# Performance work log

Hardware: AMD Instinct MI355X
Metric: run time of the kernel (lower is better)

Reference implementation:

```python
import jax, jax.numpy as jnp
import numpy as np

D = 1024   # embed_dim
L = 8      # num_blocks
H = 8      # num_heads
T = 2048   # temporal length
DH = D // H


def _ln(x, g, b, eps):
    m = jnp.mean(x, axis=-1, keepdims=True)
    v = jnp.var(x, axis=-1, keepdims=True)
    return (x - m) * jax.lax.rsqrt(v + eps) * g + b


def setup_inputs() -> dict:
    key = jax.random.key(0)
    ks = iter(jax.random.split(key, 48))
    s = 0.02
    rn = lambda shape: jax.random.normal(next(ks), shape, jnp.float32) * s
    return {
        "video_features": jax.random.normal(next(ks), (1, T, 1024), jnp.float32),
        "audio_features": jax.random.normal(next(ks), (1, T, 128), jnp.float32),
        "ap_W1": rn((128, D // 2)), "ap_b1": jnp.zeros((D // 2,)),
        "ap_W2": rn((D // 2, D)), "ap_b2": jnp.zeros((D,)),
        "vp_W1": rn((1024, D // 2)), "vp_b1": jnp.zeros((D // 2,)),
        "vp_W2": rn((D // 2, D)), "vp_b2": jnp.zeros((D,)),
        "pre_ln_g": jnp.ones((D,)), "pre_ln_b": jnp.zeros((D,)),
        "blk_Wq": rn((L, D, D)), "blk_bq": jnp.zeros((L, D)),
        "blk_Wk": rn((L, D, D)), "blk_bk": jnp.zeros((L, D)),
        "blk_Wv": rn((L, D, D)), "blk_bv": jnp.zeros((L, D)),
        "blk_Wo": rn((L, D, D)), "blk_bo": jnp.zeros((L, D)),
        "blk_bias_k": rn((L, D)), "blk_bias_v": rn((L, D)),
        "blk_ln1_g": jnp.ones((L, D)), "blk_ln1_b": jnp.zeros((L, D)),
        "blk_ln2_g": jnp.ones((L, D)), "blk_ln2_b": jnp.zeros((L, D)),
        "blk_mW1": rn((L, D, 4 * D)), "blk_mb1": jnp.zeros((L, 4 * D)),
        "blk_mW2": rn((L, 4 * D, D)), "blk_mb2": jnp.zeros((L, D)),
        "lh_W1": rn((D, D // 2)), "lh_b1": jnp.zeros((D // 2,)),
        "lh_W2": rn((D // 2, 1)), "lh_b2": jnp.zeros((1,)),
        "threshold": jnp.float32(0.5),
    }


def reference(video_features, audio_features,
              ap_W1, ap_b1, ap_W2, ap_b2,
              vp_W1, vp_b1, vp_W2, vp_b2,
              pre_ln_g, pre_ln_b,
              blk_Wq, blk_bq, blk_Wk, blk_bk, blk_Wv, blk_bv, blk_Wo, blk_bo,
              blk_bias_k, blk_bias_v,
              blk_ln1_g, blk_ln1_b, blk_ln2_g, blk_ln2_b,
              blk_mW1, blk_mb1, blk_mW2, blk_mb2,
              lh_W1, lh_b1, lh_W2, lh_b2, threshold):
    # projectors (Linear -> ReLU -> Linear)
    a = jax.nn.relu(audio_features @ ap_W1 + ap_b1) @ ap_W2 + ap_b2   # [1,T,D]
    v = jax.nn.relu(video_features @ vp_W1 + vp_b1) @ vp_W2 + vp_b2   # [1,T,D]

    x = _ln(a, pre_ln_g, pre_ln_b, 1e-6)  # pre_transformer_layer LayerNorm

    def block(x, p):
        Wq, bq, Wk, bk, Wv, bv, Wo, bo, bkx, bvx, g1, b1, g2, b2, mW1, mb1, mW2, mb2 = p
        h = _ln(x, g1, b1, 1e-5)
        q = (h @ Wq + bq).reshape(1, T, H, DH)
        # cross K/V from projected video, plus the learned bias_k/bias_v token (add_bias_kv)
        k = jnp.concatenate([v @ Wk + bk, bkx[None, None, :]], axis=1).reshape(1, T + 1, H, DH)
        val = jnp.concatenate([v @ Wv + bv, bvx[None, None, :]], axis=1).reshape(1, T + 1, H, DH)
        scores = jnp.einsum('bthd,bshd->bhts', q, k) * (DH ** -0.5)   # [1,H,T,T+1]
        attn = jax.nn.softmax(scores, axis=-1)
        o = jnp.einsum('bhts,bshd->bthd', attn, val).reshape(1, T, D)
        x = x + o @ Wo + bo
        h2 = _ln(x, g2, b2, 1e-5)
        x = x + jax.nn.gelu(h2 @ mW1 + mb1) @ mW2 + mb2
        return x, None

    ps = (blk_Wq, blk_bq, blk_Wk, blk_bk, blk_Wv, blk_bv, blk_Wo, blk_bo,
          blk_bias_k, blk_bias_v, blk_ln1_g, blk_ln1_b, blk_ln2_g, blk_ln2_b,
          blk_mW1, blk_mb1, blk_mW2, blk_mb2)
    x, _ = jax.lax.scan(block, x, ps)

    # locate head: Linear -> ReLU -> Linear -> Sigmoid
    located = jax.nn.sigmoid(jax.nn.relu(x @ lh_W1 + lh_b1) @ lh_W2 + lh_b2)[..., 0]  # [1,T]

    # on-device run-length segmentation (replaces the per-step python loop)
    clips = (located[0] > threshold).astype(jnp.int32)                 # [T]
    seg_ids = jnp.concatenate([jnp.zeros((1,), jnp.int32),
                               jnp.cumsum((clips[1:] != clips[:-1]).astype(jnp.int32))])
    counts = jax.ops.segment_sum(jnp.ones((T,), jnp.float32), seg_ids, num_segments=T)
    denom = jnp.maximum(counts, 1.0)[:, None]
    # variable-length segment mean pooling (AdaptiveAvgPool1d(1) per segment), padded to T segments
    vid_pool = jax.ops.segment_sum(v[0], seg_ids, num_segments=T) / denom   # [T,D]
    aud_pool = jax.ops.segment_sum(a[0], seg_ids, num_segments=T) / denom   # [T,D]
    seg_types = jax.ops.segment_max(clips, seg_ids, num_segments=T)
    num_seg = seg_ids[-1] + 1
    return vid_pool[None], aud_pool[None], located, seg_ids, seg_types, num_seg
```

## Files before the change

### kernel.cpp

```cpp
#include <hip/hip_runtime.h>
#include <math.h>

typedef float4 f4;
typedef __attribute__((ext_vector_type(8))) short bf8v;
typedef __attribute__((ext_vector_type(4))) float f4v;

#define T_SEQ 2048
#define D_MOD 1024

__device__ __forceinline__ float gelu_f(float x){
    float u = 0.7978845608028654f*(x + 0.044715f*x*x*x);
    return 0.5f*x*(1.0f + tanhf(u));
}

__device__ __forceinline__ unsigned f32_to_pair(float x){
    unsigned u = __float_as_uint(x);
    unsigned hi = (u + 0x7FFFu + ((u >> 16) & 1u)) >> 16;
    float hif = __uint_as_float(hi << 16);
    float lof = x - hif;
    unsigned v = __float_as_uint(lof);
    unsigned lo = (v + 0x7FFFu + ((v >> 16) & 1u)) >> 16;
    return hi | (lo << 16);
}

__device__ __forceinline__ void split2(float x, short& hi, short& lo){
    unsigned u = __float_as_uint(x);
    hi = (short)(u >> 16);
    float rem = x - __uint_as_float(u & 0xFFFF0000u);
    lo = (short)(__float_as_uint(rem) >> 16);
}

__global__ __launch_bounds__(256) void convert1(
    const float* __restrict__ s, unsigned* __restrict__ d, int n4)
{
    const int i = blockIdx.x*256 + threadIdx.x;
    if (i < n4){
        f4 v = ((const f4*)s)[i];
        uint4 o;
        o.x = f32_to_pair(v.x); o.y = f32_to_pair(v.y);
        o.z = f32_to_pair(v.z); o.w = f32_to_pair(v.w);
        ((uint4*)d)[i] = o;
    }
}

__global__ __launch_bounds__(256) void convert6(
    const float* __restrict__ s0, const float* __restrict__ s1,
    const float* __restrict__ s2, const float* __restrict__ s3,
    const float* __restrict__ s4, const float* __restrict__ s5,
    unsigned* __restrict__ d0, unsigned* __restrict__ d1,
    unsigned* __restrict__ d2, unsigned* __restrict__ d3,
    unsigned* __restrict__ d4, unsigned* __restrict__ d5)
{
    const int stride = gridDim.x * 256;
    for (int idx = blockIdx.x*256 + threadIdx.x; idx < 3145728; idx += stride){
        const float* s; unsigned* d; int off;
        if (idx < 1048576){
            const int r = idx >> 18; off = idx & 262143;
            s = (r==0)?s0:(r==1)?s1:(r==2)?s2:s3;
            d = (r==0)?d0:(r==1)?d1:(r==2)?d2:d3;
        } else if (idx < 2097152){ s = s4; d = d4; off = idx - 1048576; }
        else                     { s = s5; d = d5; off = idx - 2097152; }
        f4 v = ((const f4*)s)[off];
        uint4 o;
        o.x = f32_to_pair(v.x); o.y = f32_to_pair(v.y);
        o.z = f32_to_pair(v.z); o.w = f32_to_pair(v.w);
        ((uint4*)d)[off] = o;
    }
}

__global__ __launch_bounds__(256) void gemm_mfma(
    const unsigned* __restrict__ Apr, const unsigned* __restrict__ Wpr,
    const float* __restrict__ bias, const float* __restrict__ res,
    float* __restrict__ Cf, unsigned* __restrict__ Cp,
    int M, int N, int K, int act, int hasres, int outpair)
{
    __shared__ short Ah[2][4][64][8];
    __shared__ short Al[2][4][64][8];
    __shared__ short Bh[2][8][64][8];
    __shared__ short Bl[2][8][64][8];
    const int tid = threadIdx.x;
    const int w = tid >> 6, l = tid & 63;
    const int row0 = blockIdx.y * 64, col0 = blockIdx.x * 128;
    const int mb = (w >> 1) * 2;
    const int nb = (w & 1) * 4;

    f4v acc[2][4];
    #pragma unroll
    for (int i=0;i<2;i++)
        #pragma unroll
        for (int j=0;j<4;j++) acc[i][j] = (f4v){0.f,0.f,0.f,0.f};

    const int b_c4 = (tid & 31) * 4;
    const int b_kg = tid >> 5;

    for (int k0 = 0; k0 < K; k0 += 64){
        if (k0) __syncthreads();
        #pragma unroll
        for (int i=0;i<2;i++){
            const int u = tid + i*256;
            const int ar = u >> 3, kg = u & 7;
            const unsigned* src = Apr + (size_t)(row0 + ar)*K + k0 + kg*8;
            const uint4 p0 = *(const uint4*)src;
            const uint4 p1 = *(const uint4*)(src + 4);
            bf8v hv, lv;
            hv[0]=(short)(p0.x); lv[0]=(short)(p0.x>>16);
            hv[1]=(short)(p0.y); lv[1]=(short)(p0.y>>16);
            hv[2]=(short)(p0.z); lv[2]=(short)(p0.z>>16);
            hv[3]=(short)(p0.w); lv[3]=(short)(p0.w>>16);
            hv[4]=(short)(p1.x); lv[4]=(short)(p1.x>>16);
            hv[5]=(short)(p1.y); lv[5]=(short)(p1.y>>16);
            hv[6]=(short)(p1.z); lv[6]=(short)(p1.z>>16);
            hv[7]=(short)(p1.w); lv[7]=(short)(p1.w>>16);
            const int lane = (ar & 15) | ((kg & 3) << 4);
            const int ks = kg >> 2, mf = ar >> 4;
            *(bf8v*)&Ah[ks][mf][lane][0] = hv;
            *(bf8v*)&Al[ks][mf][lane][0] = lv;
        }
        {
            uint4 r[8];
            #pragma unroll
            for (int j=0;j<8;j++)
                r[j] = *(const uint4*)(Wpr + (size_t)(k0 + b_kg*8 + j)*N + col0 + b_c4);
            #pragma unroll
            for (int c=0;c<4;c++){
                bf8v hv, lv;
                #pragma unroll
                for (int j=0;j<8;j++){
                    const unsigned e = ((const unsigned*)&r[j])[c];
                    hv[j] = (short)e; lv[j] = (short)(e >> 16);
                }
                const int col = b_c4 + c;
                const int lane = (col & 15) | ((b_kg & 3) << 4);
                const int ks = b_kg >> 2, nf = col >> 4;
                *(bf8v*)&Bh[ks][nf][lane][0] = hv;
                *(bf8v*)&Bl[ks][nf][lane][0] = lv;
            }
        }
        __syncthreads();
        #pragma unroll
        for (int ks=0; ks<2; ks++){
            const bf8v ah0 = *(const bf8v*)&Ah[ks][mb+0][l][0];
            const bf8v ah1 = *(const bf8v*)&Ah[ks][mb+1][l][0];
            const bf8v al0 = *(const bf8v*)&Al[ks][mb+0][l][0];
            const bf8v al1 = *(const bf8v*)&Al[ks][mb+1][l][0];
            #pragma unroll
            for (int nf=0; nf<4; nf++){
                const bf8v bh = *(const bf8v*)&Bh[ks][nb+nf][l][0];
                const bf8v bl = *(const bf8v*)&Bl[ks][nb+nf][l][0];
                acc[0][nf] = __builtin_amdgcn_mfma_f32_16x16x32_bf16(ah0, bh, acc[0][nf], 0,0,0);
                acc[0][nf] = __builtin_amdgcn_mfma_f32_16x16x32_bf16(ah0, bl, acc[0][nf], 0,0,0);
                acc[0][nf] = __builtin_amdgcn_mfma_f32_16x16x32_bf16(al0, bh, acc[0][nf], 0,0,0);
                acc[1][nf] = __builtin_amdgcn_mfma_f32_16x16x32_bf16(ah1, bh, acc[1][nf], 0,0,0);
                acc[1][nf] = __builtin_amdgcn_mfma_f32_16x16x32_bf16(ah1, bl, acc[1][nf], 0,0,0);
                acc[1][nf] = __builtin_amdgcn_mfma_f32_16x16x32_bf16(al1, bh, acc[1][nf], 0,0,0);
            }
        }
    }

    const int ecol = l & 15, erow = (l >> 4) * 4;
    #pragma unroll
    for (int mf=0; mf<2; mf++){
        #pragma unroll
        for (int nf=0; nf<4; nf++){
            const int col = col0 + (w&1)*64 + nf*16 + ecol;
            const float bv = bias[col];
            #pragma unroll
            for (int j=0; j<4; j++){
                const int row = row0 + (w>>1)*32 + mf*16 + erow + j;
                float v = acc[mf][nf][j] + bv;
                if (act==1) v = fmaxf(v, 0.f);
                else if (act==2) v = gelu_f(v);
                if (hasres) v += res[(size_t)row*N + col];
                if (outpair) Cp[(size_t)row*N + col] = f32_to_pair(v);
                else         Cf[(size_t)row*N + col] = v;
            }
        }
    }
}

__global__ __launch_bounds__(512) void gemm_mfma2(
    const unsigned* __restrict__ Apr, const unsigned* __restrict__ Wpr,
    const float* __restrict__ bias, const float* __restrict__ res,
    float* __restrict__ Cf, unsigned* __restrict__ Cp,
    int M, int N, int K, int act, int hasres, int outpair)
{
    __shared__ short Ah[2][2][4][64][8];
    __shared__ short Al[2][2][4][64][8];
    __shared__ short Bh[2][2][8][64][8];
    __shared__ short Bl[2][2][8][64][8];
    const int tid = threadIdx.x;
    const int kh = tid >> 8;
    const int t  = tid & 255;
    const int w = t >> 6, l = t & 63;
    int bx = blockIdx.x, by = blockIdx.y;
    if (gridDim.x == 8 && gridDim.y == 32){
        const int flat = by*8 + bx;
        by = (flat & 7)*4 + ((flat >> 3) & 3);
        bx = flat >> 5;
    }
    const int row0 = by * 64, col0 = bx * 128;
    const int mb = (w >> 1) * 2;
    const int nb = (w & 1) * 4;
    const int K2 = K >> 1;
    const int kbase = kh * K2;
    const int b_c4 = (t & 31) * 4;
    const int b_kg = t >> 5;
    const int a_r0 = t >> 3,       a_kg0 = t & 7;
    const int a_r1 = (t+256) >> 3, a_kg1 = (t+256) & 7;

    f4v acc[2][4];
    #pragma unroll
    for (int i=0;i<2;i++)
        #pragma unroll
        for (int j=0;j<4;j++) acc[i][j] = (f4v){0.f,0.f,0.f,0.f};

    uint4 pa0[2], pa1[2], pb[8];

    {
        const unsigned* s0 = Apr + (size_t)(row0 + a_r0)*K + kbase + a_kg0*8;
        const unsigned* s1 = Apr + (size_t)(row0 + a_r1)*K + kbase + a_kg1*8;
        pa0[0] = *(const uint4*)s0; pa0[1] = *(const uint4*)(s0+4);
        pa1[0] = *(const uint4*)s1; pa1[1] = *(const uint4*)(s1+4);
        #pragma unroll
        for (int j=0;j<8;j++)
            pb[j] = *(const uint4*)(Wpr + (size_t)(kbase + b_kg*8 + j)*N + col0 + b_c4);
    }

    #define STAGE_A(pr, ar, kg) { \
        bf8v hv, lv; \
        hv[0]=(short)(pr[0].x); lv[0]=(short)(pr[0].x>>16); \
        hv[1]=(short)(pr[0].y); lv[1]=(short)(pr[0].y>>16); \
        hv[2]=(short)(pr[0].z); lv[2]=(short)(pr[0].z>>16); \
        hv[3]=(short)(pr[0].w); lv[3]=(short)(pr[0].w>>16); \
        hv[4]=(short)(pr[1].x); lv[4]=(short)(pr[1].x>>16); \
        hv[5]=(short)(pr[1].y); lv[5]=(short)(pr[1].y>>16); \
        hv[6]=(short)(pr[1].z); lv[6]=(short)(pr[1].z>>16); \
        hv[7]=(short)(pr[1].w); lv[7]=(short)(pr[1].w>>16); \
        const int lane_ = ((ar) & 15) | (((kg) & 3) << 4); \
        *(bf8v*)&Ah[kh][(kg)>>2][(ar)>>4][lane_][0] = hv; \
        *(bf8v*)&Al[kh][(kg)>>2][(ar)>>4][lane_][0] = lv; }

    #define STAGE_B() { \
        _Pragma("unroll") \
        for (int c=0;c<4;c++){ \
            bf8v hv, lv; \
            _Pragma("unroll") \
            for (int j=0;j<8;j++){ \
                const unsigned e = ((const unsigned*)&pb[j])[c]; \
                hv[j] = (short)e; lv[j] = (short)(e >> 16); \
            } \
            const int col_ = b_c4 + c; \
            const int lane_ = (col_ & 15) | ((b_kg & 3) << 4); \
            *(bf8v*)&Bh[kh][b_kg>>2][col_>>4][lane_][0] = hv; \
            *(bf8v*)&Bl[kh][b_kg>>2][col_>>4][lane_][0] = lv; } }

    STAGE_A(pa0, a_r0, a_kg0)
    STAGE_A(pa1, a_r1, a_kg1)
    STAGE_B()
    __syncthreads();

    int k0 = 0;
    while (true){
        const int kn = k0 + 64;
        const bool more = kn < K2;
        if (more){
            const unsigned* s0 = Apr + (size_t)(row0 + a_r0)*K + kbase + kn + a_kg0*8;
            const unsigned* s1 = Apr + (size_t)(row0 + a_r1)*K + kbase + kn + a_kg1*8;
            pa0[0] = *(const uint4*)s0; pa0[1] = *(const uint4*)(s0+4);
            pa1[0] = *(const uint4*)s1; pa1[1] = *(const uint4*)(s1+4);
            #pragma unroll
            for (int j=0;j<8;j++)
                pb[j] = *(const uint4*)(Wpr + (size_t)(kbase + kn + b_kg*8 + j)*N + col0 + b_c4);
        }
        #pragma unroll
        for (int ks=0; ks<2; ks++){
            const bf8v ah0 = *(const bf8v*)&Ah[kh][ks][mb+0][l][0];
            const bf8v ah1 = *(const bf8v*)&Ah[kh][ks][mb+1][l][0];
            const bf8v al0 = *(const bf8v*)&Al[kh][ks][mb+0][l][0];
            const bf8v al1 = *(const bf8v*)&Al[kh][ks][mb+1][l][0];
            #pragma unroll
            for (int nf=0; nf<4; nf++){
                const bf8v bh = *(const bf8v*)&Bh[kh][ks][nb+nf][l][0];
                const bf8v bl = *(const bf8v*)&Bl[kh][ks][nb+nf][l][0];
                acc[0][nf] = __builtin_amdgcn_mfma_f32_16x16x32_bf16(ah0, bh, acc[0][nf], 0,0,0);
                acc[0][nf] = __builtin_amdgcn_mfma_f32_16x16x32_bf16(ah0, bl, acc[0][nf], 0,0,0);
                acc[0][nf] = __builtin_amdgcn_mfma_f32_16x16x32_bf16(al0, bh, acc[0][nf], 0,0,0);
                acc[1][nf] = __builtin_amdgcn_mfma_f32_16x16x32_bf16(ah1, bh, acc[1][nf], 0,0,0);
                acc[1][nf] = __builtin_amdgcn_mfma_f32_16x16x32_bf16(ah1, bl, acc[1][nf], 0,0,0);
                acc[1][nf] = __builtin_amdgcn_mfma_f32_16x16x32_bf16(al1, bh, acc[1][nf], 0,0,0);
            }
        }
        __syncthreads();
        if (!more) break;
        STAGE_A(pa0, a_r0, a_kg0)
        STAGE_A(pa1, a_r1, a_kg1)
        STAGE_B()
        __syncthreads();
        k0 = kn;
    }

    float* cs = (float*)&Ah[0][0][0][0][0];
    if (kh == 1){
        #pragma unroll
        for (int mf=0; mf<2; mf++)
            #pragma unroll
            for (int nf=0; nf<4; nf++){
                f4 p;
                p.x=acc[mf][nf][0]; p.y=acc[mf][nf][1];
                p.z=acc[mf][nf][2]; p.w=acc[mf][nf][3];
                *(f4*)(cs + 4*(((mf*4+nf))*256 + t)) = p;
            }
    }
    __syncthreads();
    if (kh == 0){
        #pragma unroll
        for (int mf=0; mf<2; mf++)
            #pragma unroll
            for (int nf=0; nf<4; nf++){
                const f4 p = *(const f4*)(cs + 4*(((mf*4+nf))*256 + t));
                acc[mf][nf][0]+=p.x; acc[mf][nf][1]+=p.y;
                acc[mf][nf][2]+=p.z; acc[mf][nf][3]+=p.w;
            }
        const int ecol = l & 15, erow = (l >> 4) * 4;
        #pragma unroll
        for (int mf=0; mf<2; mf++){
            #pragma unroll
            for (int nf=0; nf<4; nf++){
                const int col = col0 + (w&1)*64 + nf*16 + ecol;
                const float bv = bias[col];
                #pragma unroll
                for (int j=0; j<4; j++){
                    const int row = row0 + (w>>1)*32 + mf*16 + erow + j;
                    float v = acc[mf][nf][j] + bv;
                    if (act==1) v = fmaxf(v, 0.f);
                    else if (act==2) v = gelu_f(v);
                    if (hasres) v += res[(size_t)row*N + col];
                    if (outpair) Cp[(size_t)row*N + col] = f32_to_pair(v);
                    else         Cf[(size_t)row*N + col] = v;
                }
            }
        }
    }
    #undef STAGE_A
    #undef STAGE_B
}

__global__ __launch_bounds__(512) void gemm128k2(
    const float* __restrict__ A, const float* __restrict__ W,
    const float* __restrict__ bias, const float* __restrict__ res,
    float* __restrict__ C, int M, int N, int K, int act, int hasres)
{
    __shared__ float As[2][32][68];
    __shared__ float Ws[2][32][132];
    const int tid = threadIdx.x;
    const int kh = tid >> 8;
    const int t  = tid & 255;
    const int row0 = blockIdx.y*64, col0 = blockIdx.x*128;
    const int ty = t>>4, tx = t&15;
    const int am = t>>2, ak = (t&3)*8;
    const int wk = t>>3, u  = t&7;
    const int K2 = K >> 1;
    const float* Ap = A + (size_t)(row0+am)*K + kh*K2 + ak;
    const float* Wp = W + (size_t)(kh*K2 + wk)*N + col0 + u*16;
    float* Wrow = &Ws[kh][wk][0];

    f4 a0,a1,w0,w1,w2,w3;
    a0 = *(const f4*)(Ap);
    a1 = *(const f4*)(Ap + 4);
    w0 = *(const f4*)(Wp);
    w1 = *(const f4*)(Wp + 4);
    w2 = *(const f4*)(Wp + 8);
    w3 = *(const f4*)(Wp + 12);
    As[kh][ak+0][am]=a0.x; As[kh][ak+1][am]=a0.y; As[kh][ak+2][am]=a0.z; As[kh][ak+3][am]=a0.w;
    As[kh][ak+4][am]=a1.x; As[kh][ak+5][am]=a1.y; As[kh][ak+6][am]=a1.z; As[kh][ak+7][am]=a1.w;
    *(f4*)(Wrow + 8*u)      = w0;
    *(f4*)(Wrow + 8*u + 4)  = w2;
    *(f4*)(Wrow + 64 + 8*u)     = w1;
    *(f4*)(Wrow + 64 + 8*u + 4) = w3;
    __syncthreads();

    float acc[4][8];
    #pragma unroll
    for (int i=0;i<4;i++){
        #pragma unroll
        for (int j=0;j<8;j++) acc[i][j]=0.f;
    }

    int k0 = 0;
    while (true){
        const int kn = k0 + 32;
        const bool more = kn < K2;
        if (more){
            a0 = *(const f4*)(Ap + kn);
            a1 = *(const f4*)(Ap + kn + 4);
            w0 = *(const f4*)(Wp + (size_t)kn*N);
            w1 = *(const f4*)(Wp + (size_t)kn*N + 4);
            w2 = *(const f4*)(Wp + (size_t)kn*N + 8);
            w3 = *(const f4*)(Wp + (size_t)kn*N + 12);
        }
        #pragma unroll
        for (int kk=0;kk<32;kk++){
            f4 a  = *(const f4*)&As[kh][kk][ty*4];
            f4 wA = *(const f4*)&Ws[kh][kk][tx*4];
            f4 wB = *(const f4*)&Ws[kh][kk][64 + tx*4];
            float ar[4] = {a.x,a.y,a.z,a.w};
            #pragma unroll
            for (int i=0;i<4;i++){
                acc[i][0] += ar[i]*wA.x;
                acc[i][1] += ar[i]*wA.y;
                acc[i][2] += ar[i]*wA.z;
                acc[i][3] += ar[i]*wA.w;
                acc[i][4] += ar[i]*wB.x;
                acc[i][5] += ar[i]*wB.y;
                acc[i][6] += ar[i]*wB.z;
                acc[i][7] += ar[i]*wB.w;
            }
        }
        __syncthreads();
        if (!more) break;
        As[kh][ak+0][am]=a0.x; As[kh][ak+1][am]=a0.y; As[kh][ak+2][am]=a0.z; As[kh][ak+3][am]=a0.w;
        As[kh][ak+4][am]=a1.x; As[kh][ak+5][am]=a1.y; As[kh][ak+6][am]=a1.z; As[kh][ak+7][am]=a1.w;
        *(f4*)(Wrow + 8*u)      = w0;
        *(f4*)(Wrow + 8*u + 4)  = w2;
        *(f4*)(Wrow + 64 + 8*u)     = w1;
        *(f4*)(Wrow + 64 + 8*u + 4) = w3;
        __syncthreads();
        k0 = kn;
    }

    float* cs = &Ws[0][0][0];
    if (kh == 1){
        #pragma unroll
        for (int i=0;i<4;i++){
            #pragma unroll
            for (int b=0;b<2;b++){
                f4 p;
                p.x=acc[i][b*4+0]; p.y=acc[i][b*4+1]; p.z=acc[i][b*4+2]; p.w=acc[i][b*4+3];
                *(f4*)(cs + 4*(((i<<1)|b)*256 + t)) = p;
            }
        }
    }
    __syncthreads();
    if (kh == 0){
        #pragma unroll
        for (int i=0;i<4;i++){
            #pragma unroll
            for (int b=0;b<2;b++){
                const f4 p = *(const f4*)(cs + 4*(((i<<1)|b)*256 + t));
                acc[i][b*4+0]+=p.x; acc[i][b*4+1]+=p.y; acc[i][b*4+2]+=p.z; acc[i][b*4+3]+=p.w;
            }
        }
        #pragma unroll
        for (int i=0;i<4;i++){
            const int r = row0 + ty*4 + i;
            #pragma unroll
            for (int half=0; half<2; ++half){
                const int cb = col0 + tx*8 + half*4;
                f4 bv = *(const f4*)(bias + cb);
                float t0 = acc[i][half*4+0] + bv.x;
                float t1 = acc[i][half*4+1] + bv.y;
                float t2 = acc[i][half*4+2] + bv.z;
                float t3 = acc[i][half*4+3] + bv.w;
                if (act==1){ t0=fmaxf(t0,0.f); t1=fmaxf(t1,0.f); t2=fmaxf(t2,0.f); t3=fmaxf(t3,0.f); }
                else if (act==2){ t0=gelu_f(t0); t1=gelu_f(t1); t2=gelu_f(t2); t3=gelu_f(t3); }
                if (hasres){
                    f4 rv = *(const f4*)(res + (size_t)r*N + cb);
                    t0+=rv.x; t1+=rv.y; t2+=rv.z; t3+=rv.w;
                }
                f4 o; o.x=t0; o.y=t1; o.z=t2; o.w=t3;
                *(f4*)(C + (size_t)r*N + cb) = o;
            }
        }
    }
}

__global__ __launch_bounds__(256) void lnrow(
    const float* __restrict__ X, const float* __restrict__ g,
    const float* __restrict__ b, float* __restrict__ out, float eps)
{
    __shared__ float red[4];
    const int row = blockIdx.x, tid = threadIdx.x;
    const float* xp = X + (size_t)row*D_MOD;
    f4 xv = *(const f4*)(xp + tid*4);
    float s = xv.x+xv.y+xv.z+xv.w;
    #pragma unroll
    for (int m=1;m<64;m<<=1) s += __shfl_xor(s, m);
    const int wid = tid>>6, lane = tid&63;
    if (lane==0) red[wid]=s;
    __syncthreads();
    float mean = (red[0]+red[1]+red[2]+red[3]) * (1.0f/1024.0f);
    __syncthreads();
    float d0=xv.x-mean, d1=xv.y-mean, d2=xv.z-mean, d3=xv.w-mean;
    float q = d0*d0+d1*d1+d2*d2+d3*d3;
    #pragma unroll
    for (int m=1;m<64;m<<=1) q += __shfl_xor(q, m);
    if (lane==0) red[wid]=q;
    __syncthreads();
    float var = (red[0]+red[1]+red[2]+red[3]) * (1.0f/1024.0f);
    float inv = rsqrtf(var + eps);
    f4 gv = *(const f4*)(g + tid*4);
    f4 bv = *(const f4*)(b + tid*4);
    f4 o;
    o.x = d0*inv*gv.x + bv.x;
    o.y = d1*inv*gv.y + bv.y;
    o.z = d2*inv*gv.z + bv.z;
    o.w = d3*inv*gv.w + bv.w;
    *(f4*)(out + (size_t)row*D_MOD + tid*4) = o;
}

__global__ __launch_bounds__(256) void lnrow_pair(
    const float* __restrict__ X, const float* __restrict__ g,
    const float* __restrict__ b, unsigned* __restrict__ outp, float eps)
{
    __shared__ float red[4];
    const int row = blockIdx.x, tid = threadIdx.x;
    const float* xp = X + (size_t)row*D_MOD;
    f4 xv = *(const f4*)(xp + tid*4);
    float s = xv.x+xv.y+xv.z+xv.w;
    #pragma unroll
    for (int m=1;m<64;m<<=1) s += __shfl_xor(s, m);
    const int wid = tid>>6, lane = tid&63;
    if (lane==0) red[wid]=s;
    __syncthreads();
    float mean = (red[0]+red[1]+red[2]+red[3]) * (1.0f/1024.0f);
    __syncthreads();
    float d0=xv.x-mean, d1=xv.y-mean, d2=xv.z-mean, d3=xv.w-mean;
    float q = d0*d0+d1*d1+d2*d2+d3*d3;
    #pragma unroll
    for (int m=1;m<64;m<<=1) q += __shfl_xor(q, m);
    if (lane==0) red[wid]=q;
    __syncthreads();
    float var = (red[0]+red[1]+red[2]+red[3]) * (1.0f/1024.0f);
    float inv = rsqrtf(var + eps);
    f4 gv = *(const f4*)(g + tid*4);
    f4 bv = *(const f4*)(b + tid*4);
    uint4 o;
    o.x = f32_to_pair(d0*inv*gv.x + bv.x);
    o.y = f32_to_pair(d1*inv*gv.y + bv.y);
    o.z = f32_to_pair(d2*inv*gv.z + bv.z);
    o.w = f32_to_pair(d3*inv*gv.w + bv.w);
    ((uint4*)(outp + (size_t)row*D_MOD))[tid] = o;
}

__global__ __launch_bounds__(256,1) void attn_mfma(
    const float* __restrict__ Q, const float* __restrict__ Kb,
    const float* __restrict__ Vb,
    float* __restrict__ OA0, float* __restrict__ OA1,
    float* __restrict__ ML0, float* __restrict__ ML1)
{
    __shared__ short QhS[4][8][64][8];
    __shared__ short QlS[4][8][64][8];
    __shared__ short KhS[4][4][64][8];
    __shared__ short KlS[4][4][64][8];
    __shared__ short VhS[2][8][64][8];
    __shared__ short VlS[2][8][64][8];
    short* Ph = &KhS[0][0][0][0];
    short* Pl = &KlS[0][0][0][0];

    const int tid = threadIdx.x;
    const int w = tid >> 6, l = tid & 63;
    const int h  = blockIdx.x & 7;
    const int sh = (blockIdx.x >> 3) & 1;
    const int q0 = (blockIdx.x >> 4) * 128;
    const int sbase = sh * 1024;
    const float qscale = 0.08838834764831845f;

    #pragma unroll
    for (int i=0;i<2;i++){
        const int u = tid + i*256;
        const int qr = u >> 2, dks = u & 3;
        const float* src = Q + (size_t)(q0+qr)*D_MOD + h*128 + dks*32;
        float a[32];
        #pragma unroll
        for (int j=0;j<8;j++) *(f4*)&a[j*4] = ((const f4*)src)[j];
        const int qmf = qr >> 4;
        #pragma unroll
        for (int kg=0;kg<4;kg++){
            bf8v hv, lv;
            #pragma unroll
            for (int e=0;e<8;e++){
                short hi, lo;
                split2(a[kg*8+e]*qscale, hi, lo);
                hv[e]=hi; lv[e]=lo;
            }
            const int lane = (qr & 15) | (kg << 4);
            *(bf8v*)&QhS[dks][qmf][lane][0] = hv;
            *(bf8v*)&QlS[dks][qmf][lane][0] = lv;
        }
    }
    {
        const int sr = tid >> 2, dks = tid & 3;
        const float* src = Kb + (size_t)(sbase+sr)*D_MOD + h*128 + dks*32;
        float a[32];
        #pragma unroll
        for (int j=0;j<8;j++) *(f4*)&a[j*4] = ((const f4*)src)[j];
        const int smf = sr >> 4;
        #pragma unroll
        for (int kg=0;kg<4;kg++){
            bf8v hv, lv;
            #pragma unroll
            for (int e=0;e<8;e++){ short hi,lo; split2(a[kg*8+e],hi,lo); hv[e]=hi; lv[e]=lo; }
            const int lane = (sr & 15) | (kg << 4);
            *(bf8v*)&KhS[dks][smf][lane][0] = hv;
            *(bf8v*)&KlS[dks][smf][lane][0] = lv;
        }
        const int s8 = tid >> 5, d4 = (tid & 31) * 4;
        float b[8][4];
        #pragma unroll
        for (int r=0;r<8;r++)
            *(f4*)&b[r][0] = *(const f4*)(Vb + (size_t)(sbase+s8*8+r)*D_MOD + h*128 + d4);
        const int sks = s8 >> 2, sg = s8 & 3;
        #pragma unroll
        for (int c=0;c<4;c++){
            bf8v hv, lv;
            #pragma unroll
            for (int r=0;r<8;r++){ short hi,lo; split2(b[r][c],hi,lo); hv[r]=hi; lv[r]=lo; }
            const int d = d4 + c;
            const int lane = (d & 15) | (sg << 4);
            *(bf8v*)&VhS[sks][d>>4][lane][0] = hv;
            *(bf8v*)&VlS[sks][d>>4][lane][0] = lv;
        }
    }
    __syncthreads();

    float mstat[8], lstat[8];
    f4v oacc[2][8];
    #pragma unroll
    for (int i=0;i<8;i++){ mstat[i] = -__builtin_inff(); lstat[i] = 0.f; }
    #pragma unroll
    for (int i=0;i<2;i++)
        #pragma unroll
        for (int j=0;j<8;j++) oacc[i][j] = (f4v){0.f,0.f,0.f,0.f};

    for (int t=0; t<16; ++t){
        f4v sacc[2][4];
        #pragma unroll
        for (int i=0;i<2;i++)
            #pragma unroll
            for (int j=0;j<4;j++) sacc[i][j] = (f4v){0.f,0.f,0.f,0.f};
        #pragma unroll
        for (int dks=0; dks<4; dks++){
            const bf8v qh0 = *(const bf8v*)&QhS[dks][2*w+0][l][0];
            const bf8v qh1 = *(const bf8v*)&QhS[dks][2*w+1][l][0];
            const bf8v ql0 = *(const bf8v*)&QlS[dks][2*w+0][l][0];
            const bf8v ql1 = *(const bf8v*)&QlS[dks][2*w+1][l][0];
            #pragma unroll
            for (int sf=0; sf<4; sf++){
                const bf8v kh = *(const bf8v*)&KhS[dks][sf][l][0];
                const bf8v kl = *(const bf8v*)&KlS[dks][sf][l][0];
                sacc[0][sf] = __builtin_amdgcn_mfma_f32_16x16x32_bf16(qh0, kh, sacc[0][sf], 0,0,0);
                sacc[0][sf] = __builtin_amdgcn_mfma_f32_16x16x32_bf16(qh0, kl, sacc[0][sf], 0,0,0);
                sacc[0][sf] = __builtin_amdgcn_mfma_f32_16x16x32_bf16(ql0, kh, sacc[0][sf], 0,0,0);
                sacc[1][sf] = __builtin_amdgcn_mfma_f32_16x16x32_bf16(qh1, kh, sacc[1][sf], 0,0,0);
                sacc[1][sf] = __builtin_amdgcn_mfma_f32_16x16x32_bf16(qh1, kl, sacc[1][sf], 0,0,0);
                sacc[1][sf] = __builtin_amdgcn_mfma_f32_16x16x32_bf16(ql1, kh, sacc[1][sf], 0,0,0);
            }
        }
        __syncthreads();

        float scr[8];
        #pragma unroll
        for (int mfi=0; mfi<2; mfi++){
            #pragma unroll
            for (int j=0; j<4; j++){
                const int si = mfi*4 + j;
                float tm = fmaxf(fmaxf(sacc[mfi][0][j], sacc[mfi][1][j]),
                                 fmaxf(sacc[mfi][2][j], sacc[mfi][3][j]));
                tm = fmaxf(tm, __shfl_xor(tm,1));
                tm = fmaxf(tm, __shfl_xor(tm,2));
                tm = fmaxf(tm, __shfl_xor(tm,4));
                tm = fmaxf(tm, __shfl_xor(tm,8));
                const float mn = fmaxf(mstat[si], tm);
                const float sc = __expf(mstat[si] - mn);
                float rs = 0.f;
                #pragma unroll
                for (int sf=0; sf<4; sf++){
                    const float p = __expf(sacc[mfi][sf][j] - mn);
                    sacc[mfi][sf][j] = p; rs += p;
                }
                rs += __shfl_xor(rs,1); rs += __shfl_xor(rs,2);
                rs += __shfl_xor(rs,4); rs += __shfl_xor(rs,8);
                lstat[si] = lstat[si]*sc + rs;
                mstat[si] = mn;
                scr[si] = sc;
            }
        }
        {
            const int pe = l & 7;
            const int rb4 = (l >> 4) * 4;
            const int sgb = (l & 15) >> 3;
            #pragma unroll
            for (int mfi=0; mfi<2; mfi++){
                const int qmf = 2*w + mfi;
                #pragma unroll
                for (int sf=0; sf<4; sf++){
                    const int sks = sf >> 1;
                    const int sg = (sf & 1)*2 + sgb;
                    #pragma unroll
                    for (int j=0; j<4; j++){
                        const int lane = (rb4 + j) | (sg << 4);
                        short hi, lo;
                        split2(sacc[mfi][sf][j], hi, lo);
                        const int off = ((sks*8 + qmf)*64 + lane)*8 + pe;
                        Ph[off] = hi;
                        Pl[off] = lo;
                    }
                }
            }
        }
        __syncthreads();

        #pragma unroll
        for (int mfi=0; mfi<2; mfi++){
            #pragma unroll
            for (int j=0; j<4; j++){
                const float sc = scr[mfi*4+j];
                #pragma unroll
                for (int dmf=0; dmf<8; dmf++) oacc[mfi][dmf][j] *= sc;
            }
        }
        #pragma unroll
        for (int sks=0; sks<2; sks++){
            const bf8v ph0 = *(const bf8v*)&Ph[((sks*8 + 2*w+0)*64 + l)*8];
            const bf8v ph1 = *(const bf8v*)&Ph[((sks*8 + 2*w+1)*64 + l)*8];
            const bf8v pl0 = *(const bf8v*)&Pl[((sks*8 + 2*w+0)*64 + l)*8];
            const bf8v pl1 = *(const bf8v*)&Pl[((sks*8 + 2*w+1)*64 + l)*8];
            #pragma unroll
            for (int dmf=0; dmf<8; dmf++){
                const bf8v vh = *(const bf8v*)&VhS[sks][dmf][l][0];
                const bf8v vl = *(const bf8v*)&VlS[sks][dmf][l][0];
                oacc[0][dmf] = __builtin_amdgcn_mfma_f32_16x16x32_bf16(ph0, vh, oacc[0][dmf], 0,0,0);
                oacc[0][dmf] = __builtin_amdgcn_mfma_f32_16x16x32_bf16(ph0, vl, oacc[0][dmf], 0,0,0);
                oacc[0][dmf] = __builtin_amdgcn_mfma_f32_16x16x32_bf16(pl0, vh, oacc[0][dmf], 0,0,0);
                oacc[1][dmf] = __builtin_amdgcn_mfma_f32_16x16x32_bf16(ph1, vh, oacc[1][dmf], 0,0,0);
                oacc[1][dmf] = __builtin_amdgcn_mfma_f32_16x16x32_bf16(ph1, vl, oacc[1][dmf], 0,0,0);
                oacc[1][dmf] = __builtin_amdgcn_mfma_f32_16x16x32_bf16(pl1, vh, oacc[1][dmf], 0,0,0);
            }
        }
        __syncthreads();

        if (t < 15){
            const int sb = sbase + (t+1)*64;
            const int sr = tid >> 2, dks = tid & 3;
            const float* src = Kb + (size_t)(sb+sr)*D_MOD + h*128 + dks*32;
            float a[32];
            #pragma unroll
            for (int j=0;j<8;j++) *(f4*)&a[j*4] = ((const f4*)src)[j];
            const int smf = sr >> 4;
            #pragma unroll
            for (int kg=0;kg<4;kg++){
                bf8v hv, lv;
                #pragma unroll
                for (int e=0;e<8;e++){ short hi,lo; split2(a[kg*8+e],hi,lo); hv[e]=hi; lv[e]=lo; }
                const int lane = (sr & 15) | (kg << 4);
                *(bf8v*)&KhS[dks][smf][lane][0] = hv;
                *(bf8v*)&KlS[dks][smf][lane][0] = lv;
            }
            const int s8 = tid >> 5, d4 = (tid & 31) * 4;
            float b[8][4];
            #pragma unroll
            for (int r=0;r<8;r++)
                *(f4*)&b[r][0] = *(const f4*)(Vb + (size_t)(sb+s8*8+r)*D_MOD + h*128 + d4);
            const int sks = s8 >> 2, sg = s8 & 3;
            #pragma unroll
            for (int c=0;c<4;c++){
                bf8v hv, lv;
                #pragma unroll
                for (int r=0;r<8;r++){ short hi,lo; split2(b[r][c],hi,lo); hv[r]=hi; lv[r]=lo; }
                const int d = d4 + c;
                const int lane = (d & 15) | (sg << 4);
                *(bf8v*)&VhS[sks][d>>4][lane][0] = hv;
                *(bf8v*)&VlS[sks][d>>4][lane][0] = lv;
            }
        }
        __syncthreads();
    }

    float* OAp = sh ? OA1 : OA0;
    float* MLp = sh ? ML1 : ML0;
    const int erow = (l >> 4) * 4, ecol = l & 15;
    #pragma unroll
    for (int mfi=0; mfi<2; mfi++){
        #pragma unroll
        for (int dmf=0; dmf<8; dmf++){
            const int col = h*128 + dmf*16 + ecol;
            #pragma unroll
            for (int j=0; j<4; j++){
                const int row = q0 + w*32 + mfi*16 + erow + j;
                OAp[(size_t)row*D_MOD + col] = oacc[mfi][dmf][j];
            }
        }
    }
    if (ecol == 0){
        #pragma unroll
        for (int mfi=0; mfi<2; mfi++){
            #pragma unroll
            for (int j=0; j<4; j++){
                const int row = q0 + w*32 + mfi*16 + erow + j;
                MLp[(size_t)row*16 + h*2 + 0] = mstat[mfi*4+j];
                MLp[(size_t)row*16 + h*2 + 1] = lstat[mfi*4+j];
            }
        }
    }
}

__global__ __launch_bounds__(256) void attn_combine(
    const float* __restrict__ Q, const float* __restrict__ kbias,
    const float* __restrict__ vbias,
    const float* __restrict__ OA0, const float* __restrict__ OA1,
    const float* __restrict__ ML0, const float* __restrict__ ML1,
    unsigned* __restrict__ OP)
{
    const int row = blockIdx.x, t = threadIdx.x;
    const int h = t >> 5;
    const int cc = t & 31;
    const float qscale = 0.08838834764831845f;
    const f4 qv = *(const f4*)(Q + (size_t)row*D_MOD + h*128 + cc*4);
    const f4 kb = *(const f4*)(kbias + h*128 + cc*4);
    float part = qv.x*kb.x + qv.y*kb.y + qv.z*kb.z + qv.w*kb.w;
    part += __shfl_xor(part,1); part += __shfl_xor(part,2);
    part += __shfl_xor(part,4); part += __shfl_xor(part,8);
    part += __shfl_xor(part,16);
    const float sb = part * qscale;
    const float m0 = ML0[(size_t)row*16 + h*2], l0 = ML0[(size_t)row*16 + h*2 + 1];
    const float m1 = ML1[(size_t)row*16 + h*2], l1 = ML1[(size_t)row*16 + h*2 + 1];
    const float M  = fmaxf(fmaxf(m0, m1), sb);
    const float w0 = __expf(m0 - M), w1 = __expf(m1 - M), wb = __expf(sb - M);
    const float inv = 1.0f / (w0*l0 + w1*l1 + wb);
    const f4 o0 = *(const f4*)(OA0 + (size_t)row*D_MOD + t*4);
    const f4 o1 = *(const f4*)(OA1 + (size_t)row*D_MOD + t*4);
    const f4 vb = *(const f4*)(vbias + h*128 + cc*4);
    uint4 o;
    o.x = f32_to_pair((o0.x*w0 + o1.x*w1 + vb.x*wb) * inv);
    o.y = f32_to_pair((o0.y*w0 + o1.y*w1 + vb.y*wb) * inv);
    o.z = f32_to_pair((o0.z*w0 + o1.z*w1 + vb.z*wb) * inv);
    o.w = f32_to_pair((o0.w*w0 + o1.w*w1 + vb.w*wb) * inv);
    *(uint4*)(OP + (size_t)row*D_MOD + t*4) = o;
}

__global__ __launch_bounds__(64) void locate_head(
    const float* __restrict__ mid, const float* __restrict__ W2,
    const float* __restrict__ b2, float* __restrict__ loc_ws,
    float* __restrict__ loc_out)
{
    const int row = blockIdx.x, lane = threadIdx.x;
    const float* m = mid + (size_t)row*512;
    f4 v0 = *(const f4*)(m + lane*8);
    f4 v1 = *(const f4*)(m + lane*8 + 4);
    f4 w0 = *(const f4*)(W2 + lane*8);
    f4 w1 = *(const f4*)(W2 + lane*8 + 4);
    float s = v0.x*w0.x + v0.y*w0.y + v0.z*w0.z + v0.w*w0.w
            + v1.x*w1.x + v1.y*w1.y + v1.z*w1.z + v1.w*w1.w;
    #pragma unroll
    for (int mm=1; mm<64; mm<<=1) s += __shfl_xor(s, mm);
    if (lane==0){
        float z = s + b2[0];
        float l = 1.0f/(1.0f + expf(-z));
        loc_ws[row] = l;
        loc_out[row] = l;
    }
}

__global__ __launch_bounds__(1024) void segscan(
    const float* __restrict__ located, const float* __restrict__ thrp,
    float* __restrict__ out_segid, float* __restrict__ out_segtype,
    float* __restrict__ out_numseg, int* __restrict__ wsi)
{
    __shared__ int clips[2048];
    __shared__ int segid[2048];
    __shared__ int sstart[2049];
    __shared__ int wsum[16];
    const int tid = threadIdx.x;
    const float thr = *thrp;
    for (int t=tid; t<2048; t+=1024) clips[t] = (located[t] > thr) ? 1 : 0;
    __syncthreads();
    const int t0 = tid*2, t1 = t0+1;
    int f0 = (t0==0) ? 0 : (clips[t0]!=clips[t0-1] ? 1 : 0);
    int f1 = (clips[t1]!=clips[t1-1] ? 1 : 0);
    int e0 = f0, e1 = f0+f1;
    const int lane = tid&63, wid = tid>>6;
    int v = e1;
    #pragma unroll
    for (int off=1; off<64; off<<=1){
        int u = __shfl_up(v, off, 64);
        if (lane>=off) v += u;
    }
    if (lane==63) wsum[wid] = v;
    __syncthreads();
    if (tid < 16){
        int w = wsum[tid];
        #pragma unroll
        for (int off=1; off<16; off<<=1){
            int u = __shfl_up(w, off, 16);
            if (tid>=off) w += u;
        }
        wsum[tid] = w;
    }
    __syncthreads();
    int base = (wid>0 ? wsum[wid-1] : 0) + (v - e1);
    segid[t0] = base + e0;
    segid[t1] = base + e1;
    __syncthreads();
    const int ns = segid[2047] + 1;
    for (int t=tid; t<2048; t+=1024){
        if (t==0 || segid[t]!=segid[t-1]) sstart[segid[t]] = t;
    }
    if (tid==0) sstart[ns] = 2048;
    __syncthreads();
    for (int t=tid; t<2048; t+=1024) out_segid[t] = (float)segid[t];
    for (int s=tid; s<2048; s+=1024)
        out_segtype[s] = (s<ns) ? (float)clips[sstart[s]] : -2147483648.0f;
    if (tid==0){ out_numseg[0] = (float)ns; wsi[0] = ns; }
    for (int s=tid; s<=2048; s+=1024) wsi[2+s] = (s<=ns) ? sstart[s] : 0;
}

__global__ __launch_bounds__(256) void segpool(
    const float* __restrict__ V, const float* __restrict__ A,
    const int* __restrict__ wsi, float* __restrict__ out_vid,
    float* __restrict__ out_aud)
{
    const int s = blockIdx.x;
    const int c = threadIdx.x*4;
    const int ns = wsi[0];
    f4 vv; vv.x=0.f; vv.y=0.f; vv.z=0.f; vv.w=0.f;
    f4 av = vv;
    if (s < ns){
        const int st = wsi[2+s], en = wsi[2+s+1];
        for (int r=st; r<en; ++r){
            f4 x = *(const f4*)(V + (size_t)r*D_MOD + c);
            vv.x+=x.x; vv.y+=x.y; vv.z+=x.z; vv.w+=x.w;
            f4 y = *(const f4*)(A + (size_t)r*D_MOD + c);
            av.x+=y.x; av.y+=y.y; av.z+=y.z; av.w+=y.w;
        }
        const float inv = 1.0f/(float)(en-st);
        vv.x*=inv; vv.y*=inv; vv.z*=inv; vv.w*=inv;
        av.x*=inv; av.y*=inv; av.z*=inv; av.w*=inv;
    }
    *(f4*)(out_vid + (size_t)s*D_MOD + c) = vv;
    *(f4*)(out_aud + (size_t)s*D_MOD + c) = av;
}

extern "C" void kernel_launch(void* const* d_in, const int* in_sizes, int n_in,
                              void* d_out, int out_size, void* d_ws, size_t ws_size,
                              hipStream_t stream) {
    (void)in_sizes; (void)n_in; (void)out_size; (void)ws_size;
    const float* video = (const float*)d_in[0];
    const float* audio = (const float*)d_in[1];
    const float* apW1  = (const float*)d_in[2];
    const float* apb1  = (const float*)d_in[3];
    const float* apW2  = (const float*)d_in[4];
    const float* apb2  = (const float*)d_in[5];
    const float* vpW1  = (const float*)d_in[6];
    const float* vpb1  = (const float*)d_in[7];
    const float* vpW2  = (const float*)d_in[8];
    const float* vpb2  = (const float*)d_in[9];
    const float* preg  = (const float*)d_in[10];
    const float* preb  = (const float*)d_in[11];
    const float* bWq   = (const float*)d_in[12];
    const float* bbq   = (const float*)d_in[13];
    const float* bWk   = (const float*)d_in[14];
    const float* bbk   = (const float*)d_in[15];
    const float* bWv   = (const float*)d_in[16];
    const float* bbv   = (const float*)d_in[17];
    const float* bWo   = (const float*)d_in[18];
    const float* bbo   = (const float*)d_in[19];
    const float* bbiask= (const float*)d_in[20];
    const float* bbiasv= (const float*)d_in[21];
    const float* bg1   = (const float*)d_in[22];
    const float* bb1   = (const float*)d_in[23];
    const float* bg2   = (const float*)d_in[24];
    const float* bb2   = (const float*)d_in[25];
    const float* bmW1  = (const float*)d_in[26];
    const float* bmb1  = (const float*)d_in[27];
    const float* bmW2  = (const float*)d_in[28];
    const float* bmb2  = (const float*)d_in[29];
    const float* lhW1  = (const float*)d_in[30];
    const float* lhb1  = (const float*)d_in[31];
    const float* lhW2  = (const float*)d_in[32];
    const float* lhb2  = (const float*)d_in[33];
    const float* thrp  = (const float*)d_in[34];

    float* ws = (float*)d_ws;
    float* V    = ws + 0;
    float* Abuf = ws + 2097152;
    float* X    = ws + 4194304;
    float* H    = ws + 6291456;
    float* Q    = ws + 8388608;
    float* Kb   = ws + 10485760;
    float* Vb   = ws + 12582912;
    float* Obuf = ws + 14680064;
    unsigned* M4p = (unsigned*)(ws + 8388608);
    float* M512 = ws + 16777216;
    float* LOC  = ws + 17825792;
    int*   WSI  = (int*)(ws + 17827840);
    float* ML0  = ws + 17829952;
    float* ML1  = ws + 17862720;
    unsigned* Vp  = (unsigned*)(ws + 17895488);
    unsigned* OPp = (unsigned*)(ws + 19992640);
    unsigned* WQp = (unsigned*)(ws + 22089792);
    unsigned* WKp = (unsigned*)(ws + 23138368);
    unsigned* WVp = (unsigned*)(ws + 24186944);
    unsigned* WOp = (unsigned*)(ws + 25235520);
    unsigned* W1p = (unsigned*)(ws + 26284096);
    unsigned* W2p = (unsigned*)(ws + 30478400);
    unsigned* Hp  = (unsigned*)H;

    float* out = (float*)d_out;
    float* out_vid     = out + 0;
    float* out_aud     = out + 2097152;
    float* out_loc     = out + 4194304;
    float* out_segid   = out + 4196352;
    float* out_segtype = out + 4198400;
    float* out_numseg  = out + 4200448;

    const dim3 B512(512);
    const dim3 B256(256);
    #define GRID128(M,N) dim3((N)/128,(M)/64)
    #define GRIDM(M,N)   dim3((N)/128,(M)/64)

    gemm128k2<<<GRID128(2048,512), B512, 0, stream>>>(audio, apW1, apb1, nullptr, M512, 2048,512,128, 1,0);
    gemm128k2<<<GRID128(2048,1024),B512, 0, stream>>>(M512, apW2, apb2, nullptr, Abuf, 2048,1024,512, 0,0);
    gemm128k2<<<GRID128(2048,512), B512, 0, stream>>>(video, vpW1, vpb1, nullptr, M512, 2048,512,1024, 1,0);
    gemm128k2<<<GRID128(2048,1024),B512, 0, stream>>>(M512, vpW2, vpb2, nullptr, V,    2048,1024,512, 0,0);
    lnrow<<<2048, B256, 0, stream>>>(Abuf, preg, preb, X, 1e-6f);
    convert1<<<2048, B256, 0, stream>>>(V, Vp, 524288);

    for (int l=0; l<8; ++l){
        const size_t wo = (size_t)l*1024*1024;
        const size_t bo = (size_t)l*1024;
        const size_t mo1 = (size_t)l*1024*4096;
        convert6<<<1536, B256, 0, stream>>>(bWq+wo, bWk+wo, bWv+wo, bWo+wo,
                                            bmW1+mo1, bmW2+mo1,
                                            WQp, WKp, WVp, WOp, W1p, W2p);
        lnrow_pair<<<2048, B256, 0, stream>>>(X, bg1+bo, bb1+bo, Hp, 1e-5f);
        gemm_mfma2<<<GRIDM(2048,1024), B512, 0, stream>>>(Hp, WQp, bbq+bo, nullptr, Q,  nullptr, 2048,1024,1024, 0,0,0);
        gemm_mfma2<<<GRIDM(2048,1024), B512, 0, stream>>>(Vp, WKp, bbk+bo, nullptr, Kb, nullptr, 2048,1024,1024, 0,0,0);
        gemm_mfma2<<<GRIDM(2048,1024), B512, 0, stream>>>(Vp, WVp, bbv+bo, nullptr, Vb, nullptr, 2048,1024,1024, 0,0,0);
        attn_mfma<<<256, B256, 0, stream>>>(Q, Kb, Vb, Obuf, H, ML0, ML1);
        attn_combine<<<2048, B256, 0, stream>>>(Q, bbiask+bo, bbiasv+bo, Obuf, H, ML0, ML1, OPp);
        gemm_mfma2<<<GRIDM(2048,1024), B512, 0, stream>>>(OPp, WOp, bbo+bo, X, X, nullptr, 2048,1024,1024, 0,1,0);
        lnrow_pair<<<2048, B256, 0, stream>>>(X, bg2+bo, bb2+bo, Hp, 1e-5f);
        gemm_mfma<<<GRIDM(2048,4096), B256, 0, stream>>>(Hp, W1p, bmb1+(size_t)l*4096, nullptr, nullptr, M4p, 2048,4096,1024, 2,0,1);
        gemm_mfma2<<<GRIDM(2048,1024), B512, 0, stream>>>(M4p, W2p, bmb2+bo, X, X, nullptr, 2048,1024,4096, 0,1,0);
    }

    gemm128k2<<<GRID128(2048,512), B512, 0, stream>>>(X, lhW1, lhb1, nullptr, M512, 2048,512,1024, 1,0);
    locate_head<<<2048, dim3(64), 0, stream>>>(M512, lhW2, lhb2, LOC, out_loc);
    segscan<<<1, dim3(1024), 0, stream>>>(LOC, thrp, out_segid, out_segtype, out_numseg, WSI);
    segpool<<<2048, B256, 0, stream>>>(V, Abuf, WSI, out_vid, out_aud);
}
```

Before: 4.101 ms.

## Use 64x64-tile split-K MFMA GEMM with block swizzle for MLP down-projection

```diff
diff --git a/kernel.cpp b/kernel.cpp
--- a/kernel.cpp
+++ b/kernel.cpp
@@ -343,6 +343,174 @@
     }
     #undef STAGE_A
     #undef STAGE_B
+}
+
+__global__ __launch_bounds__(512) void gemm_mfma3(
+    const unsigned* __restrict__ Apr, const unsigned* __restrict__ Wpr,
+    const float* __restrict__ bias, const float* __restrict__ res,
+    float* __restrict__ Cf, unsigned* __restrict__ Cp,
+    int M, int N, int K, int act, int hasres, int outpair)
+{
+    __shared__ short Ah[2][2][4][64][8];
+    __shared__ short Al[2][2][4][64][8];
+    __shared__ short Bh[2][2][4][64][8];
+    __shared__ short Bl[2][2][4][64][8];
+    const int tid = threadIdx.x;
+    const int kh = tid >> 8;
+    const int t  = tid & 255;
+    const int w = t >> 6, l = t & 63;
+    int bx = blockIdx.x, by = blockIdx.y;
+    if (gridDim.x == 16 && gridDim.y == 32){
+        const int flat = by*16 + bx;
+        by = (flat & 7)*4 + ((flat >> 3) & 3);
+        bx = flat >> 5;
+    }
+    const int row0 = by * 64, col0 = bx * 64;
+    const int mb = (w >> 1) * 2;
+    const int nb = (w & 1) * 2;
+    const int K2 = K >> 1;
+    const int kbase = kh * K2;
+    const int b_c2 = (t & 31) * 2;
+    const int b_kg = t >> 5;
+    const int a_r0 = t >> 3,       a_kg0 = t & 7;
+    const int a_r1 = (t+256) >> 3, a_kg1 = (t+256) & 7;
+
+    f4v acc[2][2];
+    #pragma unroll
+    for (int i=0;i<2;i++)
+        #pragma unroll
+        for (int j=0;j<2;j++) acc[i][j] = (f4v){0.f,0.f,0.f,0.f};
+
+    uint4 pa0[2], pa1[2];
+    uint2 pb[8];
+
+    {
+        const unsigned* s0 = Apr + (size_t)(row0 + a_r0)*K + kbase + a_kg0*8;
+        const unsigned* s1 = Apr + (size_t)(row0 + a_r1)*K + kbase + a_kg1*8;
+        pa0[0] = *(const uint4*)s0; pa0[1] = *(const uint4*)(s0+4);
+        pa1[0] = *(const uint4*)s1; pa1[1] = *(const uint4*)(s1+4);
+        #pragma unroll
+        for (int j=0;j<8;j++)
+            pb[j] = *(const uint2*)(Wpr + (size_t)(kbase + b_kg*8 + j)*N + col0 + b_c2);
+    }
+
+    #define STAGE_A3(pr, ar, kg) { \
+        bf8v hv, lv; \
+        hv[0]=(short)(pr[0].x); lv[0]=(short)(pr[0].x>>16); \
+        hv[1]=(short)(pr[0].y); lv[1]=(short)(pr[0].y>>16); \
+        hv[2]=(short)(pr[0].z); lv[2]=(short)(pr[0].z>>16); \
+        hv[3]=(short)(pr[0].w); lv[3]=(short)(pr[0].w>>16); \
+        hv[4]=(short)(pr[1].x); lv[4]=(short)(pr[1].x>>16); \
+        hv[5]=(short)(pr[1].y); lv[5]=(short)(pr[1].y>>16); \
+        hv[6]=(short)(pr[1].z); lv[6]=(short)(pr[1].z>>16); \
+        hv[7]=(short)(pr[1].w); lv[7]=(short)(pr[1].w>>16); \
+        const int lane_ = ((ar) & 15) | (((kg) & 3) << 4); \
+        *(bf8v*)&Ah[kh][(kg)>>2][(ar)>>4][lane_][0] = hv; \
+        *(bf8v*)&Al[kh][(kg)>>2][(ar)>>4][lane_][0] = lv; }
+
+    #define STAGE_B3() { \
+        _Pragma("unroll") \
+        for (int c=0;c<2;c++){ \
+            bf8v hv, lv; \
+            _Pragma("unroll") \
+            for (int j=0;j<8;j++){ \
+                const unsigned e = ((const unsigned*)&pb[j])[c]; \
+                hv[j] = (short)e; lv[j] = (short)(e >> 16); \
+            } \
+            const int col_ = b_c2 + c; \
+            const int lane_ = (col_ & 15) | ((b_kg & 3) << 4); \
+            *(bf8v*)&Bh[kh][b_kg>>2][col_>>4][lane_][0] = hv; \
+            *(bf8v*)&Bl[kh][b_kg>>2][col_>>4][lane_][0] = lv; } }
+
+    STAGE_A3(pa0, a_r0, a_kg0)
+    STAGE_A3(pa1, a_r1, a_kg1)
+    STAGE_B3()
+    __syncthreads();
+
+    int k0 = 0;
+    while (true){
+        const int kn = k0 + 64;
+        const bool more = kn < K2;
+        if (more){
+            const unsigned* s0 = Apr + (size_t)(row0 + a_r0)*K + kbase + kn + a_kg0*8;
+            const unsigned* s1 = Apr + (size_t)(row0 + a_r1)*K + kbase + kn + a_kg1*8;
+            pa0[0] = *(const uint4*)s0; pa0[1] = *(const uint4*)(s0+4);
+            pa1[0] = *(const uint4*)s1; pa1[1] = *(const uint4*)(s1+4);
+            #pragma unroll
+            for (int j=0;j<8;j++)
+                pb[j] = *(const uint2*)(Wpr + (size_t)(kbase + kn + b_kg*8 + j)*N + col0 + b_c2);
+        }
+        #pragma unroll
+        for (int ks=0; ks<2; ks++){
+            const bf8v ah0 = *(const bf8v*)&Ah[kh][ks][mb+0][l][0];
+            const bf8v ah1 = *(const bf8v*)&Ah[kh][ks][mb+1][l][0];
+            const bf8v al0 = *(const bf8v*)&Al[kh][ks][mb+0][l][0];
+            const bf8v al1 = *(const bf8v*)&Al[kh][ks][mb+1][l][0];
+            #pragma unroll
+            for (int nf=0; nf<2; nf++){
+                const bf8v bh = *(const bf8v*)&Bh[kh][ks][nb+nf][l][0];
+                const bf8v bl = *(const bf8v*)&Bl[kh][ks][nb+nf][l][0];
+                acc[0][nf] = __builtin_amdgcn_mfma_f32_16x16x32_bf16(ah0, bh, acc[0][nf], 0,0,0);
+                acc[0][nf] = __builtin_amdgcn_mfma_f32_16x16x32_bf16(ah0, bl, acc[0][nf], 0,0,0);
+                acc[0][nf] = __builtin_amdgcn_mfma_f32_16x16x32_bf16(al0, bh, acc[0][nf], 0,0,0);
+                acc[1][nf] = __builtin_amdgcn_mfma_f32_16x16x32_bf16(ah1, bh, acc[1][nf], 0,0,0);
+                acc[1][nf] = __builtin_amdgcn_mfma_f32_16x16x32_bf16(ah1, bl, acc[1][nf], 0,0,0);
+                acc[1][nf] = __builtin_amdgcn_mfma_f32_16x16x32_bf16(al1, bh, acc[1][nf], 0,0,0);
+            }
+        }
+        __syncthreads();
+        if (!more) break;
+        STAGE_A3(pa0, a_r0, a_kg0)
+        STAGE_A3(pa1, a_r1, a_kg1)
+        STAGE_B3()
+        __syncthreads();
+        k0 = kn;
+    }
+
+    float* cs = (float*)&Ah[0][0][0][0][0];
+    if (kh == 1){
+        #pragma unroll
+        for (int mf=0; mf<2; mf++)
+            #pragma unroll
+            for (int nf=0; nf<2; nf++){
+                f4 p;
+                p.x=acc[mf][nf][0]; p.y=acc[mf][nf][1];
+                p.z=acc[mf][nf][2]; p.w=acc[mf][nf][3];
+                *(f4*)(cs + 4*(((mf*2+nf))*256 + t)) = p;
+            }
+    }
+    __syncthreads();
+    if (kh == 0){
+        #pragma unroll
+        for (int mf=0; mf<2; mf++)
+            #pragma unroll
+            for (int nf=0; nf<2; nf++){
+                const f4 p = *(const f4*)(cs + 4*(((mf*2+nf))*256 + t));
+                acc[mf][nf][0]+=p.x; acc[mf][nf][1]+=p.y;
+                acc[mf][nf][2]+=p.z; acc[mf][nf][3]+=p.w;
+            }
+        const int ecol = l & 15, erow = (l >> 4) * 4;
+        #pragma unroll
+        for (int mf=0; mf<2; mf++){
+            #pragma unroll
+            for (int nf=0; nf<2; nf++){
+                const int col = col0 + (w&1)*32 + nf*16 + ecol;
+                const float bv = bias[col];
+                #pragma unroll
+                for (int j=0; j<4; j++){
+                    const int row = row0 + (w>>1)*32 + mf*16 + erow + j;
+                    float v = acc[mf][nf][j] + bv;
+                    if (act==1) v = fmaxf(v, 0.f);
+                    else if (act==2) v = gelu_f(v);
+                    if (hasres) v += res[(size_t)row*N + col];
+                    if (outpair) Cp[(size_t)row*N + col] = f32_to_pair(v);
+                    else         Cf[(size_t)row*N + col] = v;
+                }
+            }
+        }
+    }
+    #undef STAGE_A3
+    #undef STAGE_B3
 }
 
 __global__ __launch_bounds__(512) void gemm128k2(
@@ -1017,6 +1185,7 @@
     const dim3 B256(256);
     #define GRID128(M,N) dim3((N)/128,(M)/64)
     #define GRIDM(M,N)   dim3((N)/128,(M)/64)
+    #define GRID64(M,N)  dim3((N)/64,(M)/64)
 
     gemm128k2<<<GRID128(2048,512), B512, 0, stream>>>(audio, apW1, apb1, nullptr, M512, 2048,512,128, 1,0);
     gemm128k2<<<GRID128(2048,1024),B512, 0, stream>>>(M512, apW2, apb2, nullptr, Abuf, 2048,1024,512, 0,0);
@@ -1041,7 +1210,7 @@
         gemm_mfma2<<<GRIDM(2048,1024), B512, 0, stream>>>(OPp, WOp, bbo+bo, X, X, nullptr, 2048,1024,1024, 0,1,0);
         lnrow_pair<<<2048, B256, 0, stream>>>(X, bg2+bo, bb2+bo, Hp, 1e-5f);
         gemm_mfma<<<GRIDM(2048,4096), B256, 0, stream>>>(Hp, W1p, bmb1+(size_t)l*4096, nullptr, nullptr, M4p, 2048,4096,1024, 2,0,1);
-        gemm_mfma2<<<GRIDM(2048,1024), B512, 0, stream>>>(M4p, W2p, bmb2+bo, X, X, nullptr, 2048,1024,4096, 0,1,0);
+        gemm_mfma3<<<GRID64(2048,1024), B512, 0, stream>>>(M4p, W2p, bmb2+bo, X, X, nullptr, 2048,1024,4096, 0,1,0);
     }
 
     gemm128k2<<<GRID128(2048,512), B512, 0, stream>>>(X, lhW1, lhb1, nullptr, M512, 2048,512,1024, 1,0);
```

Result: no change. 4.072 ms (-0.7%).
